# Kernel optimization log

Measured on AMD Instinct MI355X. Metric: run time of the kernel, lower is better.

Reference implementation:

```python
import jax, jax.numpy as jnp
import numpy as np

B, S, HID = 1, 4096, 2048
NH, D = 16, 128
RATIO, TOPK, WIN = 4, 8, 128
ROPE_DIM = D // 2  # partial RoPE on first half of head_dim
EPS = 1e-6
NEG = -1e30


def rmsnorm(x, w):
    return x * jax.lax.rsqrt(jnp.mean(x * x, axis=-1, keepdims=True) + EPS) * w


def apply_rope(x, pos):
    # x: [..., L, D_head]; pos: [L] integer positions
    half = ROPE_DIM // 2
    inv = 1.0 / (10000.0 ** (jnp.arange(half, dtype=x.dtype) * (2.0 / ROPE_DIM)))
    ang = pos.astype(x.dtype)[:, None] * inv[None, :]  # [L, half]
    cos, sin = jnp.cos(ang), jnp.sin(ang)
    x1, x2, rest = x[..., :half], x[..., half:ROPE_DIM], x[..., ROPE_DIM:]
    return jnp.concatenate([x1 * cos - x2 * sin, x1 * sin + x2 * cos, rest], axis=-1)


def setup_inputs() -> dict:
    key = jax.random.key(0)
    ks = jax.random.split(key, 16)
    n = jax.random.normal
    s = 0.02
    return {
        "hidden_states": n(ks[0], (B, S, HID), jnp.float32),
        "Wq": n(ks[1], (HID, NH * D)) * s, "bq": jnp.zeros((NH * D,)),
        "Wcmp": n(ks[2], (HID, 1)) * s, "bcmp": jnp.zeros((1,)),
        "Wk": n(ks[3], (HID, D)) * s, "bk": jnp.zeros((D,)),
        "Wv": n(ks[4], (HID, D)) * s, "bv": jnp.zeros((D,)),
        "Wlk": n(ks[5], (HID, NH * D)) * s, "blk": jnp.zeros((NH * D,)),
        "Wlv": n(ks[6], (HID, NH * D)) * s, "blv": jnp.zeros((NH * D,)),
        "qn_w": jnp.ones((D,)), "kn_w": jnp.ones((D,)),
        "Wo": n(ks[7], (NH * D, HID)) * s, "bo": jnp.zeros((HID,)),
    }


def reference(hidden_states, Wq, bq, Wcmp, bcmp, Wk, bk, Wv, bv, Wlk, blk, Wlv, blv, qn_w, kn_w, Wo, bo):
    Bq, Sq, _ = hidden_states.shape
    C = Sq // RATIO
    scale = 1.0 / jnp.sqrt(jnp.float32(D))
    pos = jnp.arange(Sq)

    q = (hidden_states @ Wq + bq).reshape(Bq, Sq, NH, D).transpose(0, 2, 1, 3)  # [B,H,S,D]
    q = apply_rope(rmsnorm(q, qn_w), pos)

    # learned KV compression: softmax-weighted pooling within each block of size RATIO
    w_log = (hidden_states @ Wcmp + bcmp).reshape(Bq, C, RATIO)
    w_cmp = jax.nn.softmax(w_log, axis=-1)
    entries = jnp.einsum('bcr,bcrh->bch', w_cmp, hidden_states.reshape(Bq, C, RATIO, HID))
    block_ends = jnp.arange(1, C + 1) * RATIO - 1  # [C] last position of each block

    ck = apply_rope(rmsnorm(entries @ Wk + bk, kn_w), block_ends)  # [B,C,D] shared kv head
    cv = entries @ Wv + bv  # [B,C,D]

    # top-k block-sparse attention over compressed entries (causal on block_ends)
    sc = jnp.einsum('bhsd,bcd->bhsc', q, ck) * scale  # [B,H,S,C]
    causal = block_ends[None, None, None, :] <= pos[None, None, :, None]
    sc = jnp.where(causal, sc, NEG)
    tv, ti = jax.lax.top_k(sc, TOPK)  # [B,H,S,K]
    sel = (tv > NEG / 2).astype(sc.dtype)
    m = jnp.max(tv, axis=-1, keepdims=True)
    e = jnp.exp(tv - m) * sel
    pw = e / jnp.maximum(e.sum(axis=-1, keepdims=True), 1e-9)
    v_g = cv[jnp.arange(Bq)[:, None, None, None], ti]  # [B,H,S,K,D] irregular gather
    ctx_sparse = jnp.einsum('bhsk,bhskd->bhsd', pw, v_g)

    lk = apply_rope(rmsnorm((hidden_states @ Wlk + blk).reshape(Bq, Sq, NH, D).transpose(0, 2, 1, 3), kn_w), pos)
    lv = (hidden_states @ Wlv + blv).reshape(Bq, Sq, NH, D).transpose(0, 2, 1, 3)
    nc = Sq // WIN
    qc = q.reshape(Bq, NH, nc, WIN, D)

    def windowize(x):
        prev = jnp.pad(x, ((0, 0), (0, 0), (WIN, 0), (0, 0)))[:, :, :-WIN].reshape(Bq, NH, nc, WIN, D)
        cur = x.reshape(Bq, NH, nc, WIN, D)
        return jnp.concatenate([prev, cur], axis=3)  # [B,H,nc,2W,D]

    kw, vw = windowize(lk), windowize(lv)
    i = jnp.arange(WIN)[:, None]
    j = jnp.arange(2 * WIN)[None, :]
    rel = i + WIN - j  # qpos - kpos within the chunk pair
    band = (rel >= 0) & (rel <= WIN)
    kpos_ok = (jnp.arange(nc)[:, None, None] * WIN - WIN + j[None]) >= 0  # zero-pad chunk invalid
    mask = band[None] & kpos_ok  # [nc,W,2W]
    sl = jnp.einsum('bhcqd,bhckd->bhcqk', qc, kw) * scale
    sl = jnp.where(mask[None, None], sl, NEG)
    pl = jax.nn.softmax(sl, axis=-1)
    ctx_local = jnp.einsum('bhcqk,bhckd->bhcqd', pl, vw).reshape(Bq, NH, Sq, D)

    merged = (ctx_sparse + ctx_local) * 0.5  # mean over the two branches
    out = merged.transpose(0, 2, 1, 3).reshape(Bq, Sq, NH * D) @ Wo + bo
    return out
```

## Files before the change

### kernel.cpp

```cpp
#include <hip/hip_runtime.h>
#include <hip/hip_bf16.h>
#include <hip/hip_fp16.h>
#include <stdint.h>

typedef __hip_bfloat16 bf16;
using bf16x8 = __attribute__((ext_vector_type(8))) short;
using half8  = __attribute__((ext_vector_type(8))) _Float16;
using f32x4  = __attribute__((ext_vector_type(4))) float;

#define S_LEN   4096
#define HID_    2048
#define NH_     16
#define D_      128
#define C_      1024
#define SCALE_  0.08838834764831845f
#define DESC_   (1.0 / 1048576.0)

__device__ __forceinline__ void storeC(float* p, float v) { *p = v; }
__device__ __forceinline__ void storeC(bf16* p, float v)  { *p = __float2bfloat16(v); }
__device__ __forceinline__ void split2(float x, _Float16& h, _Float16& l) {
  h = (_Float16)x; l = (_Float16)(x - (float)h);
}
__device__ __forceinline__ short bf2s(bf16 b) { short s; __builtin_memcpy(&s, &b, 2); return s; }

#define GLDS(src, dst) __builtin_amdgcn_global_load_lds( \
    (const __attribute__((address_space(1))) void*)(src), \
    (__attribute__((address_space(3))) void*)(dst), 16, 0, 0)

__global__ __launch_bounds__(256) void cvt_bias_k(const float* __restrict__ src, bf16* __restrict__ dst,
                                                  const float* bq, const float* blk, const float* blv,
                                                  const float* bk, const float* bv, const float* bo,
                                                  float* bQ, float* bLKLV, float* bKV, float* bO) {
  int i = (blockIdx.x * 256 + threadIdx.x) * 4;
  float4 v = *(const float4*)(src + i);
  bf16 o[4] = {__float2bfloat16(v.x), __float2bfloat16(v.y),
               __float2bfloat16(v.z), __float2bfloat16(v.w)};
  *(uint2*)(dst + i) = *(uint2*)o;
  int ib = blockIdx.x * 256 + threadIdx.x;
  if (ib < 8448) {
    if (ib < 2048)      bQ[ib] = bq[ib];
    else if (ib < 6144) { int j = ib - 2048; bLKLV[j] = (j < 2048) ? blk[j] : blv[j - 2048]; }
    else if (ib < 6400) { int j = ib - 6144; bKV[j] = (j < 128) ? bk[j] : bv[j - 128]; }
    else                bO[ib - 6400] = bo[ib - 6400];
  }
}

__global__ __launch_bounds__(256) void split_q_k(const float* __restrict__ src,
                                                 _Float16* __restrict__ oh, _Float16* __restrict__ ol) {
  int i = (blockIdx.x * 256 + threadIdx.x) * 4;
  float4 v = *(const float4*)(src + i);
  float xs[4] = {v.x, v.y, v.z, v.w};
  _Float16 hh[4], ll[4];
#pragma unroll
  for (int e = 0; e < 4; ++e) split2(xs[e] * 1024.0f, hh[e], ll[e]);
  *(uint2*)(oh + i) = *(uint2*)hh;
  *(uint2*)(ol + i) = *(uint2*)ll;
}

__global__ __launch_bounds__(256) void trans_split_wq(const float* __restrict__ src,
                                                      _Float16* __restrict__ oh, _Float16* __restrict__ ol) {
  __shared__ float tile[64][65];
  const int c0 = blockIdx.x * 64, r0 = blockIdx.y * 64;
  const int t = threadIdx.x, cc = t & 63, rb = t >> 6;
#pragma unroll
  for (int i = 0; i < 16; ++i) {
    int r = rb + i * 4;
    tile[r][cc] = src[(size_t)(r0 + r) * HID_ + c0 + cc];
  }
  __syncthreads();
#pragma unroll
  for (int i = 0; i < 16; ++i) {
    int r = rb + i * 4;
    float x = tile[cc][r] * 1024.0f;
    _Float16 h, l; split2(x, h, l);
    size_t off = (size_t)(c0 + r) * HID_ + r0 + cc;
    oh[off] = h; ol[off] = l;
  }
}

__global__ __launch_bounds__(256) void transpose3_k(const float* __restrict__ Wlk, const float* __restrict__ Wlv,
                                                    const float* __restrict__ Wo,
                                                    bf16* __restrict__ bt_lklv, bf16* __restrict__ WoT) {
  __shared__ float tile[64][65];
  const float* src = (blockIdx.z == 0) ? Wlk : (blockIdx.z == 1) ? Wlv : Wo;
  bf16* dst = (blockIdx.z == 0) ? bt_lklv
            : (blockIdx.z == 1) ? (bt_lklv + (size_t)2048 * HID_) : WoT;
  const int c0 = blockIdx.x * 64, r0 = blockIdx.y * 64;
  const int t = threadIdx.x, cc = t & 63, rb = t >> 6;
#pragma unroll
  for (int i = 0; i < 16; ++i) {
    int r = rb + i * 4;
    tile[r][cc] = src[(size_t)(r0 + r) * HID_ + c0 + cc];
  }
  __syncthreads();
#pragma unroll
  for (int i = 0; i < 16; ++i) {
    int r = rb + i * 4;
    dst[(size_t)(c0 + r) * HID_ + r0 + cc] = __float2bfloat16(tile[cc][r]);
  }
}

__global__ __launch_bounds__(256) void trans_f32s_kv(const float* __restrict__ Wk, const float* __restrict__ Wv,
                                                     float* __restrict__ WkvTs) {
  __shared__ float tile[64][65];
  const float* src = blockIdx.z ? Wv : Wk;
  float* dst = WkvTs + (blockIdx.z ? (size_t)128 * HID_ : 0);
  const int c0 = blockIdx.x * 64, r0 = blockIdx.y * 64;
  const int t = threadIdx.x, cc = t & 63, rb = t >> 6;
#pragma unroll
  for (int i = 0; i < 16; ++i) {
    int r = rb + i * 4;
    tile[r][cc] = src[(size_t)(r0 + r) * 128 + c0 + cc];
  }
  __syncthreads();
#pragma unroll
  for (int i = 0; i < 16; ++i) {
    int r = rb + i * 4;
    dst[(size_t)(c0 + r) * HID_ + r0 + cc] = tile[cc][r] * 1024.0f;
  }
}

__global__ __launch_bounds__(256) void trans_v_k(const bf16* __restrict__ lklv, bf16* __restrict__ VT) {
  __shared__ ushort tile[64][65];
  const int s0 = blockIdx.x * 64, c0 = blockIdx.y * 64;
  const int t = threadIdx.x, cc = t & 63, rb = t >> 6;
  const ushort* src = (const ushort*)lklv;
#pragma unroll
  for (int i = 0; i < 16; ++i) {
    int r = rb + i * 4;
    tile[r][cc] = src[(size_t)(s0 + r) * 4096 + 2048 + c0 + cc];
  }
  __syncthreads();
  ushort* dst = (ushort*)VT;
#pragma unroll
  for (int i = 0; i < 16; ++i) {
    int r = rb + i * 4;
    dst[(size_t)(c0 + r) * 4096 + s0 + cc] = tile[cc][r];
  }
}

template <typename OutT>
__global__ __launch_bounds__(256) void gemm_bt(const bf16* __restrict__ A, const bf16* __restrict__ BT,
                                               const float* __restrict__ bias, OutT* __restrict__ Cmat,
                                               int M, int N, int K, int lda) {
  __shared__ bf16 As[128 * 32];
  __shared__ bf16 Bs[128 * 32];
  const int t = threadIdx.x;
  const int wave = t >> 6, lane = t & 63;
  const int wr = wave >> 1, wc = wave & 1;
  const int quad = lane >> 4, l15 = lane & 15;
  const int bx = blockIdx.x * 128, by = blockIdx.y * 128;
  const int srow = t >> 2, scol = (t & 3) * 8;
  f32x4 acc[4][4] = {};
  const bf16* a0 = A + (size_t)(by + srow) * lda + scol;
  const bf16* a1 = A + (size_t)(by + 64 + srow) * lda + scol;
  const bf16* b0 = BT + (size_t)(bx + srow) * K + scol;
  const bf16* b1 = BT + (size_t)(bx + 64 + srow) * K + scol;
  for (int k0 = 0; k0 < K; k0 += 32) {
    GLDS(a0 + k0, As + t * 8);
    GLDS(a1 + k0, As + 2048 + t * 8);
    GLDS(b0 + k0, Bs + t * 8);
    GLDS(b1 + k0, Bs + 2048 + t * 8);
    __syncthreads();
    bf16x8 aF[4], bF[4];
#pragma unroll
    for (int i = 0; i < 4; ++i)
      aF[i] = *(const bf16x8*)(As + (wr * 64 + i * 16 + l15) * 32 + quad * 8);
#pragma unroll
    for (int j = 0; j < 4; ++j)
      bF[j] = *(const bf16x8*)(Bs + (wc * 64 + j * 16 + l15) * 32 + quad * 8);
#pragma unroll
    for (int i = 0; i < 4; ++i)
#pragma unroll
      for (int j = 0; j < 4; ++j)
        acc[i][j] = __builtin_amdgcn_mfma_f32_16x16x32_bf16(aF[i], bF[j], acc[i][j], 0, 0, 0);
    __syncthreads();
  }
#pragma unroll
  for (int i = 0; i < 4; ++i)
#pragma unroll
    for (int j = 0; j < 4; ++j)
#pragma unroll
      for (int r = 0; r < 4; ++r) {
        int row = by + wr * 64 + i * 16 + quad * 4 + r;
        int col = bx + wc * 64 + j * 16 + l15;
        storeC(&Cmat[(size_t)row * N + col], acc[i][j][r] + bias[col]);
      }
}

__global__ __launch_bounds__(256) void gemm_hl4(const _Float16* __restrict__ Ah, const _Float16* __restrict__ Al,
                                                const _Float16* __restrict__ Bh, const _Float16* __restrict__ Bl,
                                                const float* __restrict__ bias, float* __restrict__ Cmat,
                                                int M, int N, int K, int lda) {
  __shared__ _Float16 Ahs[128 * 32], Als[128 * 32], Bhs[128 * 32], Bls[128 * 32];
  const int t = threadIdx.x;
  const int wave = t >> 6, lane = t & 63;
  const int wr = wave >> 1, wc = wave & 1;
  const int quad = lane >> 4, l15 = lane & 15;
  const int bx = blockIdx.x * 128, by = blockIdx.y * 128;
  const int srow = t >> 2, scol = (t & 3) * 8;
  double acc[4][4][4] = {};
  const _Float16* a0h = Ah + (size_t)(by + srow) * lda + scol;
  const _Float16* a1h = Ah + (size_t)(by + 64 + srow) * lda + scol;
  const _Float16* a0l = Al + (size_t)(by + srow) * lda + scol;
  const _Float16* a1l = Al + (size_t)(by + 64 + srow) * lda + scol;
  const _Float16* b0h = Bh + (size_t)(bx + srow) * K + scol;
  const _Float16* b1h = Bh + (size_t)(bx + 64 + srow) * K + scol;
  const _Float16* b0l = Bl + (size_t)(bx + srow) * K + scol;
  const _Float16* b1l = Bl + (size_t)(bx + 64 + srow) * K + scol;
  for (int k0 = 0; k0 < K; k0 += 32) {
    GLDS(a0h + k0, Ahs + t * 8);
    GLDS(a1h + k0, Ahs + 2048 + t * 8);
    GLDS(a0l + k0, Als + t * 8);
    GLDS(a1l + k0, Als + 2048 + t * 8);
    GLDS(b0h + k0, Bhs + t * 8);
    GLDS(b1h + k0, Bhs + 2048 + t * 8);
    GLDS(b0l + k0, Bls + t * 8);
    GLDS(b1l + k0, Bls + 2048 + t * 8);
    __syncthreads();
    half8 aFh[4], aFl[4], bFh[4], bFl[4];
#pragma unroll
    for (int i = 0; i < 4; ++i) {
      int ro = (wr * 64 + i * 16 + l15) * 32 + quad * 8;
      aFh[i] = *(const half8*)(Ahs + ro);
      aFl[i] = *(const half8*)(Als + ro);
    }
#pragma unroll
    for (int j = 0; j < 4; ++j) {
      int ro = (wc * 64 + j * 16 + l15) * 32 + quad * 8;
      bFh[j] = *(const half8*)(Bhs + ro);
      bFl[j] = *(const half8*)(Bls + ro);
    }
#pragma unroll
    for (int i = 0; i < 4; ++i)
#pragma unroll
      for (int j = 0; j < 4; ++j) {
        f32x4 tt = {0.f, 0.f, 0.f, 0.f};
        tt = __builtin_amdgcn_mfma_f32_16x16x32_f16(aFl[i], bFl[j], tt, 0, 0, 0);
        tt = __builtin_amdgcn_mfma_f32_16x16x32_f16(aFl[i], bFh[j], tt, 0, 0, 0);
        tt = __builtin_amdgcn_mfma_f32_16x16x32_f16(aFh[i], bFl[j], tt, 0, 0, 0);
        tt = __builtin_amdgcn_mfma_f32_16x16x32_f16(aFh[i], bFh[j], tt, 0, 0, 0);
#pragma unroll
        for (int r = 0; r < 4; ++r) acc[i][j][r] += (double)tt[r];
      }
    __syncthreads();
  }
#pragma unroll
  for (int i = 0; i < 4; ++i)
#pragma unroll
    for (int j = 0; j < 4; ++j)
#pragma unroll
      for (int r = 0; r < 4; ++r) {
        int row = by + wr * 64 + i * 16 + quad * 4 + r;
        int col = bx + wc * 64 + j * 16 + l15;
        Cmat[(size_t)row * N + col] = (float)(acc[i][j][r] * DESC_ + (double)bias[col]);
      }
}

__global__ __launch_bounds__(256) void gemm_prec4(const float* __restrict__ A, const float* __restrict__ BT,
                                                  const float* __restrict__ bias, float* __restrict__ Cmat,
                                                  int M, int N, int K, int lda) {
  __shared__ _Float16 Ah[128 * 32], Al[128 * 32], Bh[128 * 32], Bl[128 * 32];
  const int t = threadIdx.x;
  const int wave = t >> 6, lane = t & 63;
  const int wr = wave >> 1, wc = wave & 1;
  const int quad = lane >> 4, l15 = lane & 15;
  const int bx = blockIdx.x * 128, by = blockIdx.y * 128;
  double acc[4][4][4] = {};
  for (int k0 = 0; k0 < K; k0 += 32) {
#pragma unroll
    for (int it = 0; it < 4; ++it) {
      int sl = t + it * 256;
      int isB = sl >> 9, s2 = sl & 511, r = s2 >> 2, g = s2 & 3;
      const float* src = isB ? (BT + (size_t)(bx + r) * K + k0 + g * 8)
                             : (A  + (size_t)(by + r) * lda + k0 + g * 8);
      float4 u = ((const float4*)src)[0];
      float4 v = ((const float4*)src)[1];
      float xs[8] = {u.x, u.y, u.z, u.w, v.x, v.y, v.z, v.w};
      half8 hh, ll;
#pragma unroll
      for (int e = 0; e < 8; ++e) {
        float x = isB ? xs[e] : xs[e] * 1024.0f;
        _Float16 h, l; split2(x, h, l);
        hh[e] = h; ll[e] = l;
      }
      _Float16* dh = (isB ? Bh : Ah) + r * 32 + g * 8;
      _Float16* dl = (isB ? Bl : Al) + r * 32 + g * 8;
      *(half8*)dh = hh;
      *(half8*)dl = ll;
    }
    __syncthreads();
    half8 aFh[4], aFl[4], bFh[4], bFl[4];
#pragma unroll
    for (int i = 0; i < 4; ++i) {
      int ro = (wr * 64 + i * 16 + l15) * 32 + quad * 8;
      aFh[i] = *(const half8*)(Ah + ro);
      aFl[i] = *(const half8*)(Al + ro);
    }
#pragma unroll
    for (int j = 0; j < 4; ++j) {
      int ro = (wc * 64 + j * 16 + l15) * 32 + quad * 8;
      bFh[j] = *(const half8*)(Bh + ro);
      bFl[j] = *(const half8*)(Bl + ro);
    }
#pragma unroll
    for (int i = 0; i < 4; ++i)
#pragma unroll
      for (int j = 0; j < 4; ++j) {
        f32x4 tt = {0.f, 0.f, 0.f, 0.f};
        tt = __builtin_amdgcn_mfma_f32_16x16x32_f16(aFl[i], bFl[j], tt, 0, 0, 0);
        tt = __builtin_amdgcn_mfma_f32_16x16x32_f16(aFl[i], bFh[j], tt, 0, 0, 0);
        tt = __builtin_amdgcn_mfma_f32_16x16x32_f16(aFh[i], bFl[j], tt, 0, 0, 0);
        tt = __builtin_amdgcn_mfma_f32_16x16x32_f16(aFh[i], bFh[j], tt, 0, 0, 0);
#pragma unroll
        for (int r = 0; r < 4; ++r) acc[i][j][r] += (double)tt[r];
      }
    __syncthreads();
  }
#pragma unroll
  for (int i = 0; i < 4; ++i)
#pragma unroll
    for (int j = 0; j < 4; ++j)
#pragma unroll
      for (int r = 0; r < 4; ++r) {
        int row = by + wr * 64 + i * 16 + quad * 4 + r;
        int col = bx + wc * 64 + j * 16 + l15;
        Cmat[(size_t)row * N + col] = (float)(acc[i][j][r] * DESC_ + (double)bias[col]);
      }
}

__global__ __launch_bounds__(256) void normrope64_q(float* __restrict__ base, const float* __restrict__ w,
                                                    _Float16* __restrict__ qh, _Float16* __restrict__ ql) {
  __shared__ double csd[32], snd[32];
  const int s = blockIdx.x;
  const int t = threadIdx.x, wv = t >> 6, lane = t & 63;
  if (t < 32) {
    float invf = 1.0f / (float)pow(10000.0, (double)t * (1.0 / 32.0));
    float angf = (float)s * invf;
    double ang = (double)angf;
    csd[t] = cos(ang);
    snd[t] = sin(ang);
  }
  __syncthreads();
  const int fi = lane & 31;
  float* ps = base + (size_t)s * HID_;
  for (int h = wv; h < 16; h += 4) {
    float* p = ps + h * 128;
    double x0 = (double)p[lane];
    double x1 = (double)p[lane + 64];
    double ss = x0 * x0 + x1 * x1;
#pragma unroll
    for (int m = 32; m; m >>= 1) ss += __shfl_xor(ss, m, 64);
    double rstd = 1.0 / sqrt(ss * (1.0 / 128.0) + 1e-6);
    double n0 = x0 * rstd * (double)w[lane];
    double n1 = x1 * rstd * (double)w[lane + 64];
    double other = __shfl_xor(n0, 32, 64);
    double cs = csd[fi], sn = snd[fi];
    double r0 = (lane < 32) ? (n0 * cs - other * sn) : (other * sn + n0 * cs);
    float f0 = (float)r0, f1 = (float)n1;
    p[lane] = f0;
    p[lane + 64] = f1;
    _Float16 h0, l0, h1, l1;
    split2(f0 * 1024.0f, h0, l0);
    split2(f1 * 1024.0f, h1, l1);
    size_t off = (size_t)s * HID_ + h * 128;
    qh[off + lane] = h0;       ql[off + lane] = l0;
    qh[off + 64 + lane] = h1;  ql[off + 64 + lane] = l1;
  }
}

__global__ __launch_bounds__(256) void normrope64_ck(float* __restrict__ base, const float* __restrict__ w,
                                                     _Float16* __restrict__ ckh, _Float16* __restrict__ ckl) {
  int row = blockIdx.x * 4 + (threadIdx.x >> 6);
  int lane = threadIdx.x & 63;
  float* p = base + (size_t)row * 256;
  double x0 = (double)p[lane];
  double x1 = (double)p[lane + 64];
  double ss = x0 * x0 + x1 * x1;
#pragma unroll
  for (int m = 32; m; m >>= 1) ss += __shfl_xor(ss, m, 64);
  double rstd = 1.0 / sqrt(ss * (1.0 / 128.0) + 1e-6);
  double n0 = x0 * rstd * (double)w[lane];
  double n1 = x1 * rstd * (double)w[lane + 64];
  double other = __shfl_xor(n0, 32, 64);
  int fi = lane & 31;
  float invf = 1.0f / (float)pow(10000.0, (double)fi * (1.0 / 32.0));
  float angf = (float)(row * 4 + 3) * invf;
  double ang = (double)angf;
  double cs = cos(ang), sn = sin(ang);
  double r0 = (lane < 32) ? (n0 * cs - other * sn) : (other * sn + n0 * cs);
  float f0 = (float)r0, f1 = (float)n1;
  p[lane] = f0;
  p[lane + 64] = f1;
  _Float16 h0, l0, h1, l1;
  split2(f0 * 1024.0f, h0, l0);
  split2(f1 * 1024.0f, h1, l1);
  ckh[row * 128 + lane] = h0;       ckl[row * 128 + lane] = l0;
  ckh[row * 128 + 64 + lane] = h1;  ckl[row * 128 + 64 + lane] = l1;
}

__global__ __launch_bounds__(256) void normrope_bf_l(bf16* __restrict__ base, const float* __restrict__ w) {
  __shared__ float csf[32], snf[32];
  const int s = blockIdx.x;
  const int t = threadIdx.x, wv = t >> 6, lane = t & 63;
  if (t < 32) {
    float invf = 1.0f / (float)pow(10000.0, (double)t * (1.0 / 32.0));
    float ang = (float)s * invf;
    csf[t] = cosf(ang);
    snf[t] = sinf(ang);
  }
  __syncthreads();
  const int fi = lane & 31;
  bf16* ps = base + (size_t)s * 4096;
  for (int h = wv; h < 16; h += 4) {
    bf16* p = ps + h * 128;
    float x0 = __bfloat162float(p[lane]);
    float x1 = __bfloat162float(p[lane + 64]);
    float ss = x0 * x0 + x1 * x1;
#pragma unroll
    for (int m = 32; m; m >>= 1) ss += __shfl_xor(ss, m, 64);
    float rstd = rsqrtf(ss * 0.0078125f + 1e-6f);
    float n0 = x0 * rstd * w[lane];
    float n1 = x1 * rstd * w[lane + 64];
    float other = __shfl_xor(n0, 32, 64);
    float cs = csf[fi], sn = snf[fi];
    float r0 = (lane < 32) ? (n0 * cs - other * sn) : (other * sn + n0 * cs);
    p[lane] = __float2bfloat16(r0);
    p[lane + 64] = __float2bfloat16(n1);
  }
}

__global__ __launch_bounds__(256) void wlog_k(const float* __restrict__ hidden, const float* __restrict__ wcmp,
                                              const float* __restrict__ bcmp, float* __restrict__ wlog) {
  int s = blockIdx.x * 4 + (threadIdx.x >> 6);
  int lane = threadIdx.x & 63;
  const float* hp = hidden + (size_t)s * HID_;
  double acc = 0.0;
  for (int i = lane; i < HID_; i += 64)
    acc += (double)hp[i] * (double)wcmp[i];
#pragma unroll
  for (int m = 32; m; m >>= 1) acc += __shfl_xor(acc, m, 64);
  if (lane == 0) wlog[s] = (float)(acc + (double)bcmp[0]);
}

__global__ void wsm_k(const float* __restrict__ wlog, float* __restrict__ wsm) {
  int c = blockIdx.x * 256 + threadIdx.x;
  if (c >= C_) return;
  double v[4], m = -1e300;
#pragma unroll
  for (int r = 0; r < 4; ++r) { v[r] = (double)wlog[4 * c + r]; if (v[r] > m) m = v[r]; }
  double sum = 0.0;
#pragma unroll
  for (int r = 0; r < 4; ++r) { v[r] = exp(v[r] - m); sum += v[r]; }
#pragma unroll
  for (int r = 0; r < 4; ++r) wsm[4 * c + r] = (float)(v[r] / sum);
}

__global__ __launch_bounds__(256) void entries_k(const float* __restrict__ hidden, const float* __restrict__ wsm,
                                                 float* __restrict__ entriesF) {
  int idx = blockIdx.x * 256 + threadIdx.x;
  int c = idx >> 11, hcol = idx & 2047;
  double e = 0.0;
#pragma unroll
  for (int r = 0; r < 4; ++r)
    e += (double)wsm[4 * c + r] * (double)hidden[(size_t)(4 * c + r) * HID_ + hcol];
  entriesF[idx] = (float)e;
}

__global__ __launch_bounds__(1024, 8) void sparse_v9(const _Float16* __restrict__ qh, const _Float16* __restrict__ ql,
                                                     const _Float16* __restrict__ ckh, const _Float16* __restrict__ ckl,
                                                     const float* __restrict__ ckvF, bf16* __restrict__ sp) {
  __shared__ float sc[16 * 1024];
  const int by = blockIdx.y;
  const int s0 = blockIdx.x * 8;
  const int t = threadIdx.x, w = t >> 6, lane = t & 63;
  const int quad = lane >> 4, l15 = lane & 15;
  const int nvmax  = (s0 >> 2) + 2;
  const int ntiles = (nvmax + 15) >> 4;
  const double esc = (double)SCALE_ * DESC_;

  if (w < ntiles) {
    const int sA = s0 + (l15 & 7);
    const int hA = 2 * by + (l15 >> 3);
    half8 aFh[4], aFl[4];
    {
      const _Float16* qbh = qh + (size_t)sA * HID_ + hA * 128 + quad * 8;
      const _Float16* qbl = ql + (size_t)sA * HID_ + hA * 128 + quad * 8;
#pragma unroll
      for (int kk = 0; kk < 4; ++kk) {
        aFh[kk] = *(const half8*)(qbh + kk * 32);
        aFl[kk] = *(const half8*)(qbl + kk * 32);
      }
    }
    for (int ct = w; ct < ntiles; ct += 16) {
      const int c0 = ct * 16;
      const _Float16* kbh = ckh + (size_t)(c0 + l15) * 128 + quad * 8;
      const _Float16* kbl = ckl + (size_t)(c0 + l15) * 128 + quad * 8;
      double a64[4] = {0.0, 0.0, 0.0, 0.0};
#pragma unroll
      for (int kk = 0; kk < 4; ++kk) {
        half8 bh = *(const half8*)(kbh + kk * 32);
        half8 bl = *(const half8*)(kbl + kk * 32);
        f32x4 tt = {0.f, 0.f, 0.f, 0.f};
        tt = __builtin_amdgcn_mfma_f32_16x16x32_f16(aFl[kk], bl, tt, 0, 0, 0);
        tt = __builtin_amdgcn_mfma_f32_16x16x32_f16(aFl[kk], bh, tt, 0, 0, 0);
        tt = __builtin_amdgcn_mfma_f32_16x16x32_f16(aFh[kk], bl, tt, 0, 0, 0);
        tt = __builtin_amdgcn_mfma_f32_16x16x32_f16(aFh[kk], bh, tt, 0, 0, 0);
#pragma unroll
        for (int r = 0; r < 4; ++r) a64[r] += (double)tt[r];
      }
#pragma unroll
      for (int r = 0; r < 4; ++r)
        sc[(quad * 4 + r) * 1024 + c0 + l15] = (float)(a64[r] * esc);
    }
  }
  __syncthreads();
  if (w >= 4) return;

  const int q = w * 4 + quad;
  const int p2 = q >> 3, wq = q & 7;
  const int s = s0 + wq;
  const int nv = (s >= 3) ? (((s - 3) >> 2) + 1) : 0;
  const float* srow = sc + q * 1024;
  const int jmaxB = (nvmax + 63) >> 6;

  float tv0 = -1e38f, tv1 = -1e38f, tv2 = -1e38f, tv3 = -1e38f;
  int   ti0 = 0x40000000, ti1 = 0x40000000, ti2 = 0x40000000, ti3 = 0x40000000;
  for (int j = 0; j < jmaxB; ++j) {
    int cb = j * 64 + l15 * 4;
    float4 vv = *(const float4*)(srow + cb);
    float xs[4] = {vv.x, vv.y, vv.z, vv.w};
#pragma unroll
    for (int e = 0; e < 4; ++e) {
      int c = cb + e;
      float v = (c < nv) ? xs[e] : -1e38f;
      if (v > tv3) {
        if (v > tv0)      { tv3=tv2;ti3=ti2; tv2=tv1;ti2=ti1; tv1=tv0;ti1=ti0; tv0=v;ti0=c; }
        else if (v > tv1) { tv3=tv2;ti3=ti2; tv2=tv1;ti2=ti1; tv1=v;ti1=c; }
        else if (v > tv2) { tv3=tv2;ti3=ti2; tv2=v;ti2=c; }
        else              { tv3=v;ti3=c; }
      }
    }
  }

  unsigned long long deadm = 0ull;
  int ncons = 0;
  float bvs[8]; int bis[8];
#pragma unroll
  for (int it = 0; it < 8; ++it) {
    float bv = tv0; int bi = ti0;
#pragma unroll
    for (int mm = 1; mm <= 8; mm <<= 1) {
      float ov = __shfl_xor(bv, mm, 64);
      int   oi = __shfl_xor(bi, mm, 64);
      if (ov > bv || (ov == bv && oi < bi)) { bv = ov; bi = oi; }
    }
    bvs[it] = bv; bis[it] = bi;
    if (bv > -1e29f && (((bi >> 2) & 15) == l15)) {
      deadm |= 1ull << (((bi >> 6) << 2) | (bi & 3));
      tv0=tv1;ti0=ti1; tv1=tv2;ti1=ti2; tv2=tv3;ti2=ti3;
      tv3=-1e38f; ti3=0x40000000;
      if (++ncons == 4) {
        ncons = 0;
        tv0=tv1=tv2=tv3=-1e38f;
        ti0=ti1=ti2=ti3=0x40000000;
        for (int j = 0; j < jmaxB; ++j) {
          int cb = j * 64 + l15 * 4;
          float4 vv = *(const float4*)(srow + cb);
          float xs[4] = {vv.x, vv.y, vv.z, vv.w};
#pragma unroll
          for (int e = 0; e < 4; ++e) {
            int c = cb + e;
            int li = ((c >> 6) << 2) | (c & 3);
            float v = (c < nv && !((deadm >> li) & 1ull)) ? xs[e] : -1e38f;
            if (v > tv3) {
              if (v > tv0)      { tv3=tv2;ti3=ti2; tv2=tv1;ti2=ti1; tv1=tv0;ti1=ti0; tv0=v;ti0=c; }
              else if (v > tv1) { tv3=tv2;ti3=ti2; tv2=tv1;ti2=ti1; tv1=v;ti1=c; }
              else if (v > tv2) { tv3=tv2;ti3=ti2; tv2=v;ti2=c; }
              else              { tv3=v;ti3=c; }
            }
          }
        }
      }
    }
  }

  const float m0 = bvs[0];
  float a0=0.f,a1=0.f,a2=0.f,a3=0.f,a4=0.f,a5=0.f,a6=0.f,a7=0.f;
  float esum = 0.f;
#pragma unroll
  for (int it = 0; it < 8; ++it) {
    if (bvs[it] > -1e29f) {
      float wgt = expf(bvs[it] - m0);
      esum += wgt;
      const float* cvp = ckvF + (size_t)bis[it] * 256 + 128 + l15 * 8;
      float4 u = *(const float4*)cvp;
      float4 v = *(const float4*)(cvp + 4);
      a0 += wgt*u.x; a1 += wgt*u.y; a2 += wgt*u.z; a3 += wgt*u.w;
      a4 += wgt*v.x; a5 += wgt*v.y; a6 += wgt*v.z; a7 += wgt*v.w;
    }
  }
  float inv = 1.0f / fmaxf(esum, 1e-9f);
  bf16* op = sp + (size_t)s * 2048 + (2 * by + p2) * 128 + l15 * 8;
  bf16 ob[8] = {__float2bfloat16(a0*inv), __float2bfloat16(a1*inv),
                __float2bfloat16(a2*inv), __float2bfloat16(a3*inv),
                __float2bfloat16(a4*inv), __float2bfloat16(a5*inv),
                __float2bfloat16(a6*inv), __float2bfloat16(a7*inv)};
  *(uint4*)op = *(uint4*)ob;
}

__global__ __launch_bounds__(128) void local_mfma(const float* __restrict__ qf,
                                                  const bf16* __restrict__ lklv,
                                                  const bf16* __restrict__ VT,
                                                  const bf16* __restrict__ sp,
                                                  bf16* __restrict__ merged) {
  constexpr int PADP = 168;
  __shared__ bf16 PhS[2][16 * PADP];
  __shared__ bf16 PlS[2][16 * PADP];
  const int h = blockIdx.y;
// ... 15 lines not shown
#pragma unroll
      for (int e = 0; e < 8; ++e) {
        bf16 bh = __float2bfloat16(xs[e]);
        float fh = __bfloat162float(bh);
        bf16 bl = __float2bfloat16(xs[e] - fh);
        hh[e] = bf2s(bh); ll[e] = bf2s(bl);
      }
      qH[kk] = hh; qL[kk] = ll;
    }
  }

  float sc[9][4];
#pragma unroll
  for (int ct = 0; ct < 9; ++ct) {
    int key0 = kbase + ct * 16 + l15;
    const bf16* kp = lklv + (size_t)(key0 < 0 ? 0 : key0) * 4096 + h * 128 + quad * 8;
    f32x4 acc = {0.f, 0.f, 0.f, 0.f};
#pragma unroll
    for (int kk = 0; kk < 4; ++kk) {
      bf16x8 kb = *(const bf16x8*)(kp + kk * 32);
      acc = __builtin_amdgcn_mfma_f32_16x16x32_bf16(qL[kk], kb, acc, 0, 0, 0);
      acc = __builtin_amdgcn_mfma_f32_16x16x32_bf16(qH[kk], kb, acc, 0, 0, 0);
    }
#pragma unroll
    for (int r = 0; r < 4; ++r) sc[ct][r] = acc[r] * SCALE_;
  }

  float mrow[4] = {-1e30f, -1e30f, -1e30f, -1e30f};
#pragma unroll
  for (int ct = 0; ct < 9; ++ct) {
    int cidx = ct * 16 + l15;
#pragma unroll
    for (int r = 0; r < 4; ++r) {
      bool valid = (cidx >= ridx + r) && (cidx <= ridx + r + 128) && (kbase + cidx >= 0);
      float v = valid ? sc[ct][r] : -1e30f;
      sc[ct][r] = v;
      mrow[r] = fmaxf(mrow[r], v);
    }
  }
#pragma unroll
  for (int mm = 1; mm <= 8; mm <<= 1)
#pragma unroll
    for (int r = 0; r < 4; ++r) mrow[r] = fmaxf(mrow[r], __shfl_xor(mrow[r], mm, 64));

  bf16* phb = &PhS[w][0];
  bf16* plb = &PlS[w][0];
  for (int z = lane; z < 256; z += 64) {
    int zr = z >> 4, zc = z & 15;
    phb[zr * PADP + 144 + zc] = __float2bfloat16(0.f);
    plb[zr * PADP + 144 + zc] = __float2bfloat16(0.f);
  }
  float lsum[4] = {0.f, 0.f, 0.f, 0.f};
#pragma unroll
  for (int ct = 0; ct < 9; ++ct) {
    int cidx = ct * 16 + l15;
#pragma unroll
    for (int r = 0; r < 4; ++r) {
      float e = (sc[ct][r] > -1e29f) ? expf(sc[ct][r] - mrow[r]) : 0.f;
      lsum[r] += e;
      bf16 bh = __float2bfloat16(e);
      float fh = __bfloat162float(bh);
      bf16 bl = __float2bfloat16(e - fh);
      phb[(ridx + r) * PADP + cidx] = bh;
      plb[(ridx + r) * PADP + cidx] = bl;
    }
  }
#pragma unroll
  for (int mm = 1; mm <= 8; mm <<= 1)
#pragma unroll
    for (int r = 0; r < 4; ++r) lsum[r] += __shfl_xor(lsum[r], mm, 64);
  float inv[4];
#pragma unroll
  for (int r = 0; r < 4; ++r) inv[r] = 1.0f / lsum[r];

  bf16x8 pH[5], pL[5];
#pragma unroll
  for (int kk = 0; kk < 5; ++kk) {
    pH[kk] = *(const bf16x8*)(phb + l15 * PADP + kk * 32 + quad * 8);
    pL[kk] = *(const bf16x8*)(plb + l15 * PADP + kk * 32 + quad * 8);
  }

#pragma unroll
  for (int dt = 0; dt < 8; ++dt) {
    const bf16* vrow = VT + (size_t)(h * 128 + dt * 16 + l15) * 4096;
    f32x4 acc = {0.f, 0.f, 0.f, 0.f};
#pragma unroll
    for (int kk = 0; kk < 5; ++kk) {
      int ko = kbase + kk * 32 + quad * 8;
      ko = ko < 0 ? 0 : (ko > 4088 ? 4088 : ko);
      bf16x8 vb = *(const bf16x8*)(vrow + ko);
      acc = __builtin_amdgcn_mfma_f32_16x16x32_bf16(pL[kk], vb, acc, 0, 0, 0);
      acc = __builtin_amdgcn_mfma_f32_16x16x32_bf16(pH[kk], vb, acc, 0, 0, 0);
    }
#pragma unroll
    for (int r = 0; r < 4; ++r) {
      int srow = sw + ridx + r;
      size_t off = (size_t)srow * 2048 + h * 128 + dt * 16 + l15;
      float spv = __bfloat162float(sp[off]);
      merged[off] = __float2bfloat16((acc[r] * inv[r] + spv) * 0.5f);
    }
  }
}

extern "C" void kernel_launch(void* const* d_in, const int* in_sizes, int n_in,
                              void* d_out, int out_size, void* d_ws, size_t ws_size,
                              hipStream_t stream) {
  (void)in_sizes; (void)n_in; (void)out_size; (void)ws_size;
  const float* hidden = (const float*)d_in[0];
  const float* Wq   = (const float*)d_in[1];
  const float* bq   = (const float*)d_in[2];
  const float* Wcmp = (const float*)d_in[3];
  const float* bcmp = (const float*)d_in[4];
  const float* Wk   = (const float*)d_in[5];
  const float* bk   = (const float*)d_in[6];
  const float* Wv   = (const float*)d_in[7];
  const float* bv   = (const float*)d_in[8];
  const float* Wlk  = (const float*)d_in[9];
  const float* blk  = (const float*)d_in[10];
  const float* Wlv  = (const float*)d_in[11];
  const float* blv  = (const float*)d_in[12];
  const float* qn_w = (const float*)d_in[13];
  const float* kn_w = (const float*)d_in[14];
  const float* Wo   = (const float*)d_in[15];
  const float* bo   = (const float*)d_in[16];
  float* out = (float*)d_out;

  char* ws = (char*)d_ws;
  float*    qf       = (float*)   (ws);
  bf16*     lklv     = (bf16*)    (ws + 33554432);
  _Float16* qh       = (_Float16*)(ws + 67108864);
  bf16*     VT       = (bf16*)    (ws + 67108864);
  bf16*     hbf      = (bf16*)    (ws + 83886080);
  _Float16* hidh     = (_Float16*)(ws + 83886080);
  bf16*     merged   = (bf16*)    (ws + 83886080);
  bf16*     bt_lklv  = (bf16*)    (ws + 100663296);
  _Float16* hidl     = (_Float16*)(ws + 100663296);
  bf16*     sp       = (bf16*)    (ws + 100663296);
  float*    WkvTs    = (float*)   (ws + 117440512);
  bf16*     WoT      = (bf16*)    (ws + 119537664);
  float*    entriesF = (float*)   (ws + 127926272);
  float*    ckvF     = (float*)   (ws + 136314880);
  _Float16* ckh      = (_Float16*)(ws + 137363456);
  _Float16* ckl      = (_Float16*)(ws + 137625600);
  float*    wlog     = (float*)   (ws + 137887744);
  float*    wsm      = (float*)   (ws + 137904128);
  float*    bQ       = (float*)   (ws + 137920512);
  float*    bLKLV    = (float*)   (ws + 137928704);
  float*    bKV      = (float*)   (ws + 137945088);
  float*    bO       = (float*)   (ws + 137946112);
  _Float16* wqh      = (_Float16*)(ws + 137954304);
  _Float16* wql      = (_Float16*)(ws + 146342912);
  _Float16* ql       = (_Float16*)(ws + 137954304);

  cvt_bias_k<<<dim3(8192), dim3(256), 0, stream>>>(hidden, hbf, bq, blk, blv, bk, bv, bo,
                                                   bQ, bLKLV, bKV, bO);
  transpose3_k<<<dim3(32, 32, 3), dim3(256), 0, stream>>>(Wlk, Wlv, Wo, bt_lklv, WoT);
  trans_f32s_kv<<<dim3(2, 32, 2), dim3(256), 0, stream>>>(Wk, Wv, WkvTs);

  wlog_k<<<dim3(1024), dim3(256), 0, stream>>>(hidden, Wcmp, bcmp, wlog);
  wsm_k<<<dim3(4), dim3(256), 0, stream>>>(wlog, wsm);
  entries_k<<<dim3(8192), dim3(256), 0, stream>>>(hidden, wsm, entriesF);

  gemm_bt<bf16><<<dim3(32, 32), dim3(256), 0, stream>>>(hbf, bt_lklv, bLKLV, lklv, S_LEN, 4096, HID_, HID_);
  gemm_prec4<<<dim3(2, 8), dim3(256), 0, stream>>>(entriesF, WkvTs, bKV, ckvF, C_, 256, HID_, HID_);

  split_q_k<<<dim3(8192), dim3(256), 0, stream>>>(hidden, hidh, hidl);
  trans_split_wq<<<dim3(32, 32), dim3(256), 0, stream>>>(Wq, wqh, wql);
  gemm_hl4<<<dim3(16, 32), dim3(256), 0, stream>>>(hidh, hidl, wqh, wql, bQ, qf, S_LEN, HID_, HID_, HID_);

  normrope64_q<<<dim3(4096), dim3(256), 0, stream>>>(qf, qn_w, qh, ql);
  normrope64_ck<<<dim3(256), dim3(256), 0, stream>>>(ckvF, kn_w, ckh, ckl);
  normrope_bf_l<<<dim3(4096), dim3(256), 0, stream>>>(lklv, kn_w);

  sparse_v9<<<dim3(512, 8), dim3(1024), 0, stream>>>(qh, ql, ckh, ckl, ckvF, sp);
  trans_v_k<<<dim3(64, 32), dim3(256), 0, stream>>>(lklv, VT);
  local_mfma<<<dim3(128, 16), dim3(128), 0, stream>>>(qf, lklv, VT, sp, merged);

  gemm_bt<float><<<dim3(16, 32), dim3(256), 0, stream>>>(merged, WoT, bO, out, S_LEN, HID_, HID_, HID_);
}
```

Baseline: 1.040 ms.

## Merge independent prep, GEMM and norm-rope kernels into block-indexed fused launches

Independent kernels are merged into shared launches that branch on the block index: weight transposes, bf16 conversion and wlog go into one prep kernel; the LK/LV GEMM shares a launch with entries pooling; Q and CKV GEMMs share one; the three norm-rope kernels share one. This cuts the launch count and lets small tail-heavy kernels (the 16-block CKV GEMM, the norm-rope passes) overlap with bigger ones instead of running serially. The cost is that shared-memory and register allocation take the maximum over the fused branches, which can lower occupancy, and the heterogeneous blocks may balance poorly.

```diff
diff --git a/kernel.cpp b/kernel.cpp
--- a/kernel.cpp
+++ b/kernel.cpp
@@ -27,16 +27,17 @@
     (const __attribute__((address_space(1))) void*)(src), \
     (__attribute__((address_space(3))) void*)(dst), 16, 0, 0)
 
-__global__ __launch_bounds__(256) void cvt_bias_k(const float* __restrict__ src, bf16* __restrict__ dst,
-                                                  const float* bq, const float* blk, const float* blv,
-                                                  const float* bk, const float* bv, const float* bo,
-                                                  float* bQ, float* bLKLV, float* bKV, float* bO) {
-  int i = (blockIdx.x * 256 + threadIdx.x) * 4;
+
+__device__ __forceinline__ void cvt_bias_body(int bxx, const float* __restrict__ src, bf16* __restrict__ dst,
+                                              const float* bq, const float* blk, const float* blv,
+                                              const float* bk, const float* bv, const float* bo,
+                                              float* bQ, float* bLKLV, float* bKV, float* bO) {
+  int i = (bxx * 256 + threadIdx.x) * 4;
   float4 v = *(const float4*)(src + i);
   bf16 o[4] = {__float2bfloat16(v.x), __float2bfloat16(v.y),
                __float2bfloat16(v.z), __float2bfloat16(v.w)};
   *(uint2*)(dst + i) = *(uint2*)o;
-  int ib = blockIdx.x * 256 + threadIdx.x;
+  int ib = bxx * 256 + threadIdx.x;
   if (ib < 8448) {
     if (ib < 2048)      bQ[ib] = bq[ib];
     else if (ib < 6144) { int j = ib - 2048; bLKLV[j] = (j < 2048) ? blk[j] : blv[j - 2048]; }
@@ -45,9 +46,67 @@
   }
 }
 
-__global__ __launch_bounds__(256) void split_q_k(const float* __restrict__ src,
-                                                 _Float16* __restrict__ oh, _Float16* __restrict__ ol) {
-  int i = (blockIdx.x * 256 + threadIdx.x) * 4;
+__device__ __forceinline__ void transpose3_body(int bxx, int byy, int bzz, char* smem,
+                                                const float* __restrict__ Wlk, const float* __restrict__ Wlv,
+                                                const float* __restrict__ Wo,
+                                                bf16* __restrict__ bt_lklv, bf16* __restrict__ WoT) {
+  float (*tile)[65] = (float(*)[65])smem;
+  const float* src = (bzz == 0) ? Wlk : (bzz == 1) ? Wlv : Wo;
+  bf16* dst = (bzz == 0) ? bt_lklv
+            : (bzz == 1) ? (bt_lklv + (size_t)2048 * HID_) : WoT;
+  const int c0 = bxx * 64, r0 = byy * 64;
+  const int t = threadIdx.x, cc = t & 63, rb = t >> 6;
+#pragma unroll
+  for (int i = 0; i < 16; ++i) {
+    int r = rb + i * 4;
+    tile[r][cc] = src[(size_t)(r0 + r) * HID_ + c0 + cc];
+  }
+  __syncthreads();
+#pragma unroll
+  for (int i = 0; i < 16; ++i) {
+    int r = rb + i * 4;
+    dst[(size_t)(c0 + r) * HID_ + r0 + cc] = __float2bfloat16(tile[cc][r]);
+  }
+}
+
+__device__ __forceinline__ void trans_kv_body(int bxx, int byy, int bzz, char* smem,
+                                              const float* __restrict__ Wk, const float* __restrict__ Wv,
+                                              float* __restrict__ WkvTs) {
+  float (*tile)[65] = (float(*)[65])smem;
+  const float* src = bzz ? Wv : Wk;
+  float* dst = WkvTs + (bzz ? (size_t)128 * HID_ : 0);
+  const int c0 = bxx * 64, r0 = byy * 64;
+  const int t = threadIdx.x, cc = t & 63, rb = t >> 6;
+#pragma unroll
+  for (int i = 0; i < 16; ++i) {
+    int r = rb + i * 4;
+    tile[r][cc] = src[(size_t)(r0 + r) * 128 + c0 + cc];
+  }
+  __syncthreads();
+#pragma unroll
+  for (int i = 0; i < 16; ++i) {
+    int r = rb + i * 4;
+    dst[(size_t)(c0 + r) * HID_ + r0 + cc] = tile[cc][r] * 1024.0f;
+  }
+}
+
+__device__ __forceinline__ void wlog_body(int bxx, const float* __restrict__ hidden,
+                                          const float* __restrict__ wcmp, const float* __restrict__ bcmp,
+                                          float* __restrict__ wlog) {
+  int s = bxx * 4 + (threadIdx.x >> 6);
+  int lane = threadIdx.x & 63;
+  const float* hp = hidden + (size_t)s * HID_;
+  double acc = 0.0;
+  for (int i = lane; i < HID_; i += 64)
+    acc += (double)hp[i] * (double)wcmp[i];
+#pragma unroll
+  for (int m = 32; m; m >>= 1) acc += __shfl_xor(acc, m, 64);
+  if (lane == 0) wlog[s] = (float)(acc + (double)bcmp[0]);
+}
+
+__device__ __forceinline__ void split_q_body(int bxx, const float* __restrict__ src,
+                                             _Float16* __restrict__ oh, _Float16* __restrict__ ol) {
+  int i = (bxx * 256 + threadIdx.x) * 4;
   float4 v = *(const float4*)(src + i);
   float xs[4] = {v.x, v.y, v.z, v.w};
   _Float16 hh[4], ll[4];
@@ -57,10 +116,11 @@
   *(uint2*)(ol + i) = *(uint2*)ll;
 }
 
-__global__ __launch_bounds__(256) void trans_split_wq(const float* __restrict__ src,
-                                                      _Float16* __restrict__ oh, _Float16* __restrict__ ol) {
-  __shared__ float tile[64][65];
-  const int c0 = blockIdx.x * 64, r0 = blockIdx.y * 64;
+__device__ __forceinline__ void trans_split_wq_body(int bxx, int byy, char* smem,
+                                                    const float* __restrict__ src,
+                                                    _Float16* __restrict__ oh, _Float16* __restrict__ ol) {
+  float (*tile)[65] = (float(*)[65])smem;
+  const int c0 = bxx * 64, r0 = byy * 64;
   const int t = threadIdx.x, cc = t & 63, rb = t >> 6;
 #pragma unroll
   for (int i = 0; i < 16; ++i) {
@@ -78,78 +138,27 @@
   }
 }
 
-__global__ __launch_bounds__(256) void transpose3_k(const float* __restrict__ Wlk, const float* __restrict__ Wlv,
-                                                    const float* __restrict__ Wo,
-                                                    bf16* __restrict__ bt_lklv, bf16* __restrict__ WoT) {
-  __shared__ float tile[64][65];
-  const float* src = (blockIdx.z == 0) ? Wlk : (blockIdx.z == 1) ? Wlv : Wo;
-  bf16* dst = (blockIdx.z == 0) ? bt_lklv
-            : (blockIdx.z == 1) ? (bt_lklv + (size_t)2048 * HID_) : WoT;
-  const int c0 = blockIdx.x * 64, r0 = blockIdx.y * 64;
-  const int t = threadIdx.x, cc = t & 63, rb = t >> 6;
-#pragma unroll
-  for (int i = 0; i < 16; ++i) {
-    int r = rb + i * 4;
-    tile[r][cc] = src[(size_t)(r0 + r) * HID_ + c0 + cc];
-  }
-  __syncthreads();
-#pragma unroll
-  for (int i = 0; i < 16; ++i) {
-    int r = rb + i * 4;
-    dst[(size_t)(c0 + r) * HID_ + r0 + cc] = __float2bfloat16(tile[cc][r]);
-  }
-}
-
-__global__ __launch_bounds__(256) void trans_f32s_kv(const float* __restrict__ Wk, const float* __restrict__ Wv,
-                                                     float* __restrict__ WkvTs) {
-  __shared__ float tile[64][65];
-  const float* src = blockIdx.z ? Wv : Wk;
-  float* dst = WkvTs + (blockIdx.z ? (size_t)128 * HID_ : 0);
-  const int c0 = blockIdx.x * 64, r0 = blockIdx.y * 64;
-  const int t = threadIdx.x, cc = t & 63, rb = t >> 6;
-#pragma unroll
-  for (int i = 0; i < 16; ++i) {
-    int r = rb + i * 4;
-    tile[r][cc] = src[(size_t)(r0 + r) * 128 + c0 + cc];
-  }
-  __syncthreads();
-#pragma unroll
-  for (int i = 0; i < 16; ++i) {
-    int r = rb + i * 4;
-    dst[(size_t)(c0 + r) * HID_ + r0 + cc] = tile[cc][r] * 1024.0f;
-  }
-}
-
-__global__ __launch_bounds__(256) void trans_v_k(const bf16* __restrict__ lklv, bf16* __restrict__ VT) {
-  __shared__ ushort tile[64][65];
-  const int s0 = blockIdx.x * 64, c0 = blockIdx.y * 64;
-  const int t = threadIdx.x, cc = t & 63, rb = t >> 6;
-  const ushort* src = (const ushort*)lklv;
-#pragma unroll
-  for (int i = 0; i < 16; ++i) {
-    int r = rb + i * 4;
-    tile[r][cc] = src[(size_t)(s0 + r) * 4096 + 2048 + c0 + cc];
-  }
-  __syncthreads();
-  ushort* dst = (ushort*)VT;
-#pragma unroll
-  for (int i = 0; i < 16; ++i) {
-    int r = rb + i * 4;
-    dst[(size_t)(c0 + r) * 4096 + s0 + cc] = tile[cc][r];
-  }
+__device__ __forceinline__ void entries_body(int bxx, const float* __restrict__ hidden,
+                                             const float* __restrict__ wsm, float* __restrict__ entriesF) {
+  int idx = bxx * 256 + threadIdx.x;
+  int c = idx >> 11, hcol = idx & 2047;
+  double e = 0.0;
+#pragma unroll
+  for (int r = 0; r < 4; ++r)
+    e += (double)wsm[4 * c + r] * (double)hidden[(size_t)(4 * c + r) * HID_ + hcol];
+  entriesF[idx] = (float)e;
 }
 
 template <typename OutT>
-__global__ __launch_bounds__(256) void gemm_bt(const bf16* __restrict__ A, const bf16* __restrict__ BT,
-                                               const float* __restrict__ bias, OutT* __restrict__ Cmat,
-                                               int M, int N, int K, int lda) {
-  __shared__ bf16 As[128 * 32];
-  __shared__ bf16 Bs[128 * 32];
+__device__ __forceinline__ void gemm_bt_body(int bxp, int byp, bf16* As, bf16* Bs,
+                                             const bf16* __restrict__ A, const bf16* __restrict__ BT,
+                                             const float* __restrict__ bias, OutT* __restrict__ Cmat,
+                                             int M, int N, int K, int lda) {
   const int t = threadIdx.x;
   const int wave = t >> 6, lane = t & 63;
   const int wr = wave >> 1, wc = wave & 1;
   const int quad = lane >> 4, l15 = lane & 15;
-  const int bx = blockIdx.x * 128, by = blockIdx.y * 128;
+  const int bx = bxp * 128, by = byp * 128;
   const int srow = t >> 2, scol = (t & 3) * 8;
   f32x4 acc[4][4] = {};
   const bf16* a0 = A + (size_t)(by + srow) * lda + scol;
@@ -188,16 +197,17 @@
       }
 }
 
-__global__ __launch_bounds__(256) void gemm_hl4(const _Float16* __restrict__ Ah, const _Float16* __restrict__ Al,
-                                                const _Float16* __restrict__ Bh, const _Float16* __restrict__ Bl,
-                                                const float* __restrict__ bias, float* __restrict__ Cmat,
-                                                int M, int N, int K, int lda) {
-  __shared__ _Float16 Ahs[128 * 32], Als[128 * 32], Bhs[128 * 32], Bls[128 * 32];
+__device__ __forceinline__ void gemm_hl4_body(int bxp, int byp, _Float16* Ahs, _Float16* Als,
+                                              _Float16* Bhs, _Float16* Bls,
+                                              const _Float16* __restrict__ Ah, const _Float16* __restrict__ Al,
+                                              const _Float16* __restrict__ Bh, const _Float16* __restrict__ Bl,
+                                              const float* __restrict__ bias, float* __restrict__ Cmat,
+                                              int M, int N, int K, int lda) {
   const int t = threadIdx.x;
   const int wave = t >> 6, lane = t & 63;
   const int wr = wave >> 1, wc = wave & 1;
   const int quad = lane >> 4, l15 = lane & 15;
-  const int bx = blockIdx.x * 128, by = blockIdx.y * 128;
+  const int bx = bxp * 128, by = byp * 128;
   const int srow = t >> 2, scol = (t & 3) * 8;
   double acc[4][4][4] = {};
   const _Float16* a0h = Ah + (size_t)(by + srow) * lda + scol;
@@ -257,15 +267,16 @@
       }
 }
 
-__global__ __launch_bounds__(256) void gemm_prec4(const float* __restrict__ A, const float* __restrict__ BT,
-                                                  const float* __restrict__ bias, float* __restrict__ Cmat,
-                                                  int M, int N, int K, int lda) {
-  __shared__ _Float16 Ah[128 * 32], Al[128 * 32], Bh[128 * 32], Bl[128 * 32];
+__device__ __forceinline__ void gemm_prec4_body(int bxp, int byp, _Float16* Ah, _Float16* Al,
+                                                _Float16* Bh, _Float16* Bl,
+                                                const float* __restrict__ A, const float* __restrict__ BT,
+                                                const float* __restrict__ bias, float* __restrict__ Cmat,
+                                                int M, int N, int K, int lda) {
   const int t = threadIdx.x;
   const int wave = t >> 6, lane = t & 63;
   const int wr = wave >> 1, wc = wave & 1;
   const int quad = lane >> 4, l15 = lane & 15;
-  const int bx = blockIdx.x * 128, by = blockIdx.y * 128;
+  const int bx = bxp * 128, by = byp * 128;
   double acc[4][4][4] = {};
   for (int k0 = 0; k0 < K; k0 += 32) {
 #pragma unroll
@@ -329,10 +340,9 @@
       }
 }
 
-__global__ __launch_bounds__(256) void normrope64_q(float* __restrict__ base, const float* __restrict__ w,
-                                                    _Float16* __restrict__ qh, _Float16* __restrict__ ql) {
-  __shared__ double csd[32], snd[32];
-  const int s = blockIdx.x;
+__device__ __forceinline__ void normrope_q_body(int s, double* csd, double* snd,
+                                                float* __restrict__ base, const float* __restrict__ w,
+                                                _Float16* __restrict__ qh, _Float16* __restrict__ ql) {
   const int t = threadIdx.x, wv = t >> 6, lane = t & 63;
   if (t < 32) {
     float invf = 1.0f / (float)pow(10000.0, (double)t * (1.0 / 32.0));
@@ -369,9 +379,9 @@
   }
 }
 
-__global__ __launch_bounds__(256) void normrope64_ck(float* __restrict__ base, const float* __restrict__ w,
-                                                     _Float16* __restrict__ ckh, _Float16* __restrict__ ckl) {
-  int row = blockIdx.x * 4 + (threadIdx.x >> 6);
+__device__ __forceinline__ void normrope_ck_body(int bxx, float* __restrict__ base, const float* __restrict__ w,
+                                                 _Float16* __restrict__ ckh, _Float16* __restrict__ ckl) {
+  int row = bxx * 4 + (threadIdx.x >> 6);
   int lane = threadIdx.x & 63;
   float* p = base + (size_t)row * 256;
   double x0 = (double)p[lane];
@@ -399,9 +409,8 @@
   ckh[row * 128 + 64 + lane] = h1;  ckl[row * 128 + 64 + lane] = l1;
 }
 
-__global__ __launch_bounds__(256) void normrope_bf_l(bf16* __restrict__ base, const float* __restrict__ w) {
-  __shared__ float csf[32], snf[32];
-  const int s = blockIdx.x;
+__device__ __forceinline__ void normrope_bfl_body(int s, float* csf, float* snf,
+                                                  bf16* __restrict__ base, const float* __restrict__ w) {
   const int t = threadIdx.x, wv = t >> 6, lane = t & 63;
   if (t < 32) {
     float invf = 1.0f / (float)pow(10000.0, (double)t * (1.0 / 32.0));
@@ -430,17 +439,28 @@
   }
 }
 
-__global__ __launch_bounds__(256) void wlog_k(const float* __restrict__ hidden, const float* __restrict__ wcmp,
-                                              const float* __restrict__ bcmp, float* __restrict__ wlog) {
-  int s = blockIdx.x * 4 + (threadIdx.x >> 6);
-  int lane = threadIdx.x & 63;
-  const float* hp = hidden + (size_t)s * HID_;
-  double acc = 0.0;
-  for (int i = lane; i < HID_; i += 64)
-    acc += (double)hp[i] * (double)wcmp[i];
-#pragma unroll
-  for (int m = 32; m; m >>= 1) acc += __shfl_xor(acc, m, 64);
-  if (lane == 0) wlog[s] = (float)(acc + (double)bcmp[0]);
+
+__global__ __launch_bounds__(256) void prep_fused(const float* hidden, bf16* hbf,
+                                                  const float* Wlk, const float* Wlv, const float* Wo,
+                                                  bf16* bt_lklv, bf16* WoT,
+                                                  const float* Wk, const float* Wv, float* WkvTs,
+                                                  const float* wcmp, const float* bcmp, float* wlog,
+                                                  const float* bq, const float* blk, const float* blv,
+                                                  const float* bk, const float* bv, const float* bo,
+                                                  float* bQ, float* bLKLV, float* bKV, float* bO) {
+  __shared__ __align__(16) char smem[16640];
+  int b = blockIdx.x;
+  if (b < 3072) {
+    int z = b >> 10, rem = b & 1023;
+    transpose3_body(rem & 31, rem >> 5, z, smem, Wlk, Wlv, Wo, bt_lklv, WoT);
+  } else if (b < 3200) {
+    int tt = b - 3072;
+    trans_kv_body(tt & 1, (tt & 63) >> 1, tt >> 6, smem, Wk, Wv, WkvTs);
+  } else if (b < 11392) {
+    cvt_bias_body(b - 3200, hidden, hbf, bq, blk, blv, bk, bv, bo, bQ, bLKLV, bKV, bO);
+  } else {
+    wlog_body(b - 11392, hidden, wcmp, bcmp, wlog);
+  }
 }
 
 __global__ void wsm_k(const float* __restrict__ wlog, float* __restrict__ wsm) {
@@ -456,15 +476,90 @@
   for (int r = 0; r < 4; ++r) wsm[4 * c + r] = (float)(v[r] / sum);
 }
 
-__global__ __launch_bounds__(256) void entries_k(const float* __restrict__ hidden, const float* __restrict__ wsm,
-                                                 float* __restrict__ entriesF) {
-  int idx = blockIdx.x * 256 + threadIdx.x;
-  int c = idx >> 11, hcol = idx & 2047;
-  double e = 0.0;
-#pragma unroll
-  for (int r = 0; r < 4; ++r)
-    e += (double)wsm[4 * c + r] * (double)hidden[(size_t)(4 * c + r) * HID_ + hcol];
-  entriesF[idx] = (float)e;
+__global__ __launch_bounds__(256) void lklv_entries_fused(const bf16* hbf, const bf16* bt_lklv,
+                                                          const float* bLKLV, bf16* lklv,
+                                                          const float* hidden, const float* wsm,
+                                                          float* entriesF) {
+  __shared__ __align__(16) bf16 AsBs[2][4096];
+  int b = blockIdx.x;
+  if (b < 1024) {
+    gemm_bt_body<bf16>(b & 31, b >> 5, AsBs[0], AsBs[1], hbf, bt_lklv, bLKLV, lklv,
+                       S_LEN, 4096, HID_, HID_);
+  } else {
+    entries_body(b - 1024, hidden, wsm, entriesF);
+  }
+}
+
+__global__ __launch_bounds__(256) void splitq_fused(const float* hidden, _Float16* hidh, _Float16* hidl,
+                                                    const float* Wq, _Float16* wqh, _Float16* wql) {
+  __shared__ __align__(16) char smem[16640];
+  int b = blockIdx.x;
+  if (b < 1024) {
+    trans_split_wq_body(b & 31, b >> 5, smem, Wq, wqh, wql);
+  } else {
+    split_q_body(b - 1024, hidden, hidh, hidl);
+  }
+}
+
+__global__ __launch_bounds__(256) void qgemm_fused(const _Float16* hidh, const _Float16* hidl,
+                                                   const _Float16* wqh, const _Float16* wql,
+                                                   const float* bQ, float* qf,
+                                                   const float* entriesF, const float* WkvTs,
+                                                   const float* bKV, float* ckvF) {
+  __shared__ __align__(16) _Float16 SH4[4][4096];
+  int b = blockIdx.x;
+  if (b < 512) {
+    gemm_hl4_body(b & 15, b >> 4, SH4[0], SH4[1], SH4[2], SH4[3],
+                  hidh, hidl, wqh, wql, bQ, qf, S_LEN, HID_, HID_, HID_);
+  } else {
+    int tt = b - 512;
+    gemm_prec4_body(tt & 1, tt >> 1, SH4[0], SH4[1], SH4[2], SH4[3],
+                    entriesF, WkvTs, bKV, ckvF, C_, 256, HID_, HID_);
+  }
+}
+
+__global__ __launch_bounds__(256) void normrope_fused(float* qf, const float* qn_w,
+                                                      _Float16* qh, _Float16* ql,
+                                                      float* ckvF, const float* kn_w,
+                                                      _Float16* ckh, _Float16* ckl,
+                                                      bf16* lklv) {
+  __shared__ double csd[32], snd[32];
+  __shared__ float csf[32], snf[32];
+  int b = blockIdx.x;
+  if (b < 256) {
+    normrope_ck_body(b, ckvF, kn_w, ckh, ckl);
+  } else if (b < 4352) {
+    normrope_q_body(b - 256, csd, snd, qf, qn_w, qh, ql);
+  } else {
+    normrope_bfl_body(b - 4352, csf, snf, lklv, kn_w);
+  }
+}
+
+__global__ __launch_bounds__(256) void trans_v_k(const bf16* __restrict__ lklv, bf16* __restrict__ VT) {
+  __shared__ ushort tile[64][65];
+  const int s0 = blockIdx.x * 64, c0 = blockIdx.y * 64;
+  const int t = threadIdx.x, cc = t & 63, rb = t >> 6;
+  const ushort* src = (const ushort*)lklv;
+#pragma unroll
+  for (int i = 0; i < 16; ++i) {
+    int r = rb + i * 4;
+    tile[r][cc] = src[(size_t)(s0 + r) * 4096 + 2048 + c0 + cc];
+  }
+  __syncthreads();
+  ushort* dst = (ushort*)VT;
+#pragma unroll
+  for (int i = 0; i < 16; ++i) {
+    int r = rb + i * 4;
+    dst[(size_t)(c0 + r) * 4096 + s0 + cc] = tile[cc][r];
+  }
+}
+
+template <typename OutT>
+__global__ __launch_bounds__(256) void gemm_bt(const bf16* __restrict__ A, const bf16* __restrict__ BT,
+                                               const float* __restrict__ bias, OutT* __restrict__ Cmat,
+                                               int M, int N, int K, int lda) {
+  __shared__ __align__(16) bf16 AsBs[2][4096];
+  gemm_bt_body<OutT>(blockIdx.x, blockIdx.y, AsBs[0], AsBs[1], A, BT, bias, Cmat, M, N, K, lda);
 }
 
 __global__ __launch_bounds__(1024, 8) void sparse_v9(const _Float16* __restrict__ qh, const _Float16* __restrict__ ql,
@@ -786,29 +881,18 @@
   _Float16* wql      = (_Float16*)(ws + 146342912);
   _Float16* ql       = (_Float16*)(ws + 137954304);
 
-  cvt_bias_k<<<dim3(8192), dim3(256), 0, stream>>>(hidden, hbf, bq, blk, blv, bk, bv, bo,
-                                                   bQ, bLKLV, bKV, bO);
-  transpose3_k<<<dim3(32, 32, 3), dim3(256), 0, stream>>>(Wlk, Wlv, Wo, bt_lklv, WoT);
-  trans_f32s_kv<<<dim3(2, 32, 2), dim3(256), 0, stream>>>(Wk, Wv, WkvTs);
-
-  wlog_k<<<dim3(1024), dim3(256), 0, stream>>>(hidden, Wcmp, bcmp, wlog);
+  prep_fused<<<dim3(12416), dim3(256), 0, stream>>>(hidden, hbf, Wlk, Wlv, Wo, bt_lklv, WoT,
+                                                    Wk, Wv, WkvTs, Wcmp, bcmp, wlog,
+                                                    bq, blk, blv, bk, bv, bo, bQ, bLKLV, bKV, bO);
   wsm_k<<<dim3(4), dim3(256), 0, stream>>>(wlog, wsm);
-  entries_k<<<dim3(8192), dim3(256), 0, stream>>>(hidden, wsm, entriesF);
-
-  gemm_bt<bf16><<<dim3(32, 32), dim3(256), 0, stream>>>(hbf, bt_lklv, bLKLV, lklv, S_LEN, 4096, HID_, HID_);
-  gemm_prec4<<<dim3(2, 8), dim3(256), 0, stream>>>(entriesF, WkvTs, bKV, ckvF, C_, 256, HID_, HID_);
-
-  split_q_k<<<dim3(8192), dim3(256), 0, stream>>>(hidden, hidh, hidl);
-  trans_split_wq<<<dim3(32, 32), dim3(256), 0, stream>>>(Wq, wqh, wql);
-  gemm_hl4<<<dim3(16, 32), dim3(256), 0, stream>>>(hidh, hidl, wqh, wql, bQ, qf, S_LEN, HID_, HID_, HID_);
-
-  normrope64_q<<<dim3(4096), dim3(256), 0, stream>>>(qf, qn_w, qh, ql);
-  normrope64_ck<<<dim3(256), dim3(256), 0, stream>>>(ckvF, kn_w, ckh, ckl);
-  normrope_bf_l<<<dim3(4096), dim3(256), 0, stream>>>(lklv, kn_w);
-
+  lklv_entries_fused<<<dim3(9216), dim3(256), 0, stream>>>(hbf, bt_lklv, bLKLV, lklv,
+                                                           hidden, wsm, entriesF);
+  splitq_fused<<<dim3(9216), dim3(256), 0, stream>>>(hidden, hidh, hidl, Wq, wqh, wql);
+  qgemm_fused<<<dim3(528), dim3(256), 0, stream>>>(hidh, hidl, wqh, wql, bQ, qf,
+                                                   entriesF, WkvTs, bKV, ckvF);
+  normrope_fused<<<dim3(8448), dim3(256), 0, stream>>>(qf, qn_w, qh, ql, ckvF, kn_w, ckh, ckl, lklv);
   sparse_v9<<<dim3(512, 8), dim3(1024), 0, stream>>>(qh, ql, ckh, ckl, ckvF, sp);
   trans_v_k<<<dim3(64, 32), dim3(256), 0, stream>>>(lklv, VT);
   local_mfma<<<dim3(128, 16), dim3(128), 0, stream>>>(qf, lklv, VT, sp, merged);
-
   gemm_bt<float><<<dim3(16, 32), dim3(256), 0, stream>>>(merged, WoT, bO, out, S_LEN, HID_, HID_, HID_);
 }
```

Result: faster. 997.7 us (-4.1%).
